# Performance work log

Hardware: AMD Instinct MI355X
Metric: run time of the kernel (lower is better)

## Reference

```python
import jax, jax.numpy as jnp
import numpy as np

N_NODES = 100000
N_REL = 500
DIM = 200
N_EDGES = 200000
T_STEPS = 3
EPS = 1e-12


def _l2norm(x):
    # F.normalize(x): L2 along last dim with eps clamp
    n = jnp.sqrt(jnp.sum(x * x, axis=-1, keepdims=True))
    return x / jnp.maximum(n, EPS)


def _rgcn_layer(h, r, src, rel, dst, W_msg, W_loop):
    # UnionRGCN layer: msg = (h[src] + r[rel]) @ W_msg, mean-aggregated at dst,
    # plus self-loop transform. No activation (active=False), dropout=0.
    msg = (h[src] + r[rel]) @ W_msg                      # [E, D]
    deg = jax.ops.segment_sum(jnp.ones((src.shape[0],), h.dtype), dst,
                              num_segments=N_NODES)       # [N]
    agg = jax.ops.segment_sum(msg, dst, num_segments=N_NODES)
    agg = agg / jnp.maximum(deg, 1.0)[:, None]
    return agg + h @ W_loop


def setup_inputs() -> dict:
    key = jax.random.key(0)
    ks = jax.random.split(key, 10)
    edge_list = []
    for t in range(T_STEPS):
        kt = jax.random.fold_in(ks[0], t)
        k1, k2, k3 = jax.random.split(kt, 3)
        src = jax.random.randint(k1, (N_EDGES,), 0, N_NODES)
        rel = jax.random.randint(k2, (N_EDGES,), 0, N_REL)
        dst = jax.random.randint(k3, (N_EDGES,), 0, N_NODES)
        edge_list.append(jnp.stack([src, rel, dst], axis=1))
    edges = jnp.stack(edge_list)  # [T, E, 3]
    s = 1.0 / np.sqrt(DIM)
    return {
        "edges": edges,
        "entity_embed": jax.random.normal(ks[1], (N_NODES, DIM), jnp.float32),
        "relation_embed": jax.random.normal(ks[2], (N_REL, DIM), jnp.float32),
        "W_msg1": jax.random.normal(ks[3], (DIM, DIM), jnp.float32) * s,
        "W_loop1": jax.random.normal(ks[4], (DIM, DIM), jnp.float32) * s,
        "W_msg2": jax.random.normal(ks[5], (DIM, DIM), jnp.float32) * s,
        "W_loop2": jax.random.normal(ks[6], (DIM, DIM), jnp.float32) * s,
        "time_gate_weight": jax.random.normal(ks[7], (DIM, DIM), jnp.float32) * s * np.sqrt(2.0),
        "time_gate_bias": jnp.zeros((DIM,), jnp.float32),
    }


def reference(edges, entity_embed, relation_embed, W_msg1, W_loop1, W_msg2,
              W_loop2, time_gate_weight, time_gate_bias):
    h = _l2norm(entity_embed)
    r = _l2norm(relation_embed)
    for t in range(T_STEPS):  # small fixed temporal loop, as in source
        src, rel, dst = edges[t, :, 0], edges[t, :, 1], edges[t, :, 2]
        cur = _rgcn_layer(h, r, src, rel, dst, W_msg1, W_loop1)
        cur = _rgcn_layer(cur, r, src, rel, dst, W_msg2, W_loop2)
        cur = _l2norm(cur)
        gate = jax.nn.sigmoid(h @ time_gate_weight + time_gate_bias)
        h = _l2norm(gate * cur + (1.0 - gate) * h)
    return h
```

## Files before the change

kernel.cpp:

```cpp
#include <hip/hip_runtime.h>
#include <math.h>

#define DIMN   200
#define NNODES 100000
#define NREL   500
#define NEDGES 200000
#define KSTEPS 7
#define NB16   16
#define WPK_ELEMS (KSTEPS * NB16 * 64 * 8)
#define SCAN_B 1024
#define NBN    6252
#define FRAG_STRIDE 3584

typedef float  v4f  __attribute__((ext_vector_type(4)));
typedef __bf16 v8bf __attribute__((ext_vector_type(8)));

__device__ __forceinline__ size_t frag_chunk(int nb, int c, int r) {
    return (size_t)(nb * KSTEPS + (c >> 2)) * 512 + (size_t)((c & 3) * 128 + r * 8);
}

__launch_bounds__(256)
__global__ void l2norm_pro(const float* __restrict__ in, __bf16* __restrict__ outR,
                           __bf16* __restrict__ outF, int nrows)
{
    int idx  = blockIdx.x * 256 + threadIdx.x;
    int node = idx >> 5;
    int ch   = idx & 31;
    if (node >= nrows) return;
    float v[8] = {};
    if (ch < 25) {
        const float4* p = (const float4*)(in + (size_t)node * DIMN + ch * 8);
        float4 f0 = p[0], f1 = p[1];
        v[0]=f0.x; v[1]=f0.y; v[2]=f0.z; v[3]=f0.w;
        v[4]=f1.x; v[5]=f1.y; v[6]=f1.z; v[7]=f1.w;
    }
    float ss = 0.0f;
    #pragma unroll
    for (int k = 0; k < 8; ++k) ss += v[k] * v[k];
    #pragma unroll
    for (int off = 16; off; off >>= 1) ss += __shfl_xor(ss, off, 64);
    float s = 1.0f / fmaxf(sqrtf(ss), 1e-12f);
    #pragma unroll
    for (int k = 0; k < 8; ++k) v[k] *= s;
    if (ch < 25) {
        v8bf o;
        #pragma unroll
        for (int k = 0; k < 8; ++k) o[k] = (__bf16)v[k];
        *(v8bf*)(outR + (size_t)node * DIMN + ch * 8) = o;
    }
    if (outF && ch < 28) {
        v8bf o;
        #pragma unroll
        for (int k = 0; k < 8; ++k) o[k] = (ch < 25) ? (__bf16)v[k] : (__bf16)0.0f;
        *(v8bf*)(outF + frag_chunk(node >> 4, ch, node & 15)) = o;
    }
}

__launch_bounds__(256)
__global__ void edge_hist(const int* __restrict__ edges, int* __restrict__ counts, int nedges)
{
    int e = blockIdx.x * 256 + threadIdx.x;
    if (e < nedges) atomicAdd(&counts[edges[e * 3 + 2]], 1);
}

__launch_bounds__(SCAN_B)
__global__ void scan1(const int* __restrict__ counts, int* __restrict__ tmp,
                      int* __restrict__ bsum, int n)
{
    __shared__ int sh[SCAN_B];
    int i = blockIdx.x * SCAN_B + threadIdx.x;
    int v = (i < n) ? counts[i] : 0;
    sh[threadIdx.x] = v;
    __syncthreads();
    for (int off = 1; off < SCAN_B; off <<= 1) {
        int t = (threadIdx.x >= off) ? sh[threadIdx.x - off] : 0;
        __syncthreads();
        sh[threadIdx.x] += t;
        __syncthreads();
    }
    if (i < n) tmp[i] = sh[threadIdx.x];
    if (threadIdx.x == SCAN_B - 1) bsum[blockIdx.x] = sh[threadIdx.x];
}

__launch_bounds__(128)
__global__ void scan2(int* __restrict__ bsum, int nb)
{
    __shared__ int sh[128];
    int v = (threadIdx.x < nb) ? bsum[threadIdx.x] : 0;
    sh[threadIdx.x] = v;
    __syncthreads();
    for (int off = 1; off < 128; off <<= 1) {
        int t = (threadIdx.x >= off) ? sh[threadIdx.x - off] : 0;
        __syncthreads();
        sh[threadIdx.x] += t;
        __syncthreads();
    }
    if (threadIdx.x < nb) bsum[threadIdx.x] = sh[threadIdx.x] - v;
}

__launch_bounds__(SCAN_B)
__global__ void scan3(const int* __restrict__ tmp, const int* __restrict__ bsum,
                      int* __restrict__ offs, int n)
{
    int i = blockIdx.x * SCAN_B + threadIdx.x;
    if (i < n) offs[i + 1] = tmp[i] + bsum[blockIdx.x];
    if (i == 0) offs[0] = 0;
}

__launch_bounds__(256)
__global__ void edge_fill(const int* __restrict__ edges, const int* __restrict__ offs,
                          int* __restrict__ cursor, int2* __restrict__ sorted, int nedges)
{
    int e = blockIdx.x * 256 + threadIdx.x;
    if (e >= nedges) return;
    int s = edges[e * 3 + 0];
    int r = edges[e * 3 + 1];
    int d = edges[e * 3 + 2];
    int p = offs[d] + atomicAdd(&cursor[d], 1);
    sorted[p] = make_int2(s, r);
}

__launch_bounds__(256)
__global__ void agg_S(const int* __restrict__ offs, const int2* __restrict__ sorted,
                      const __bf16* __restrict__ XR, const __bf16* __restrict__ RnR,
                      __bf16* __restrict__ SF, int nnodes)
{
    int wave = (int)((blockIdx.x * blockDim.x + threadIdx.x) >> 6);
    int lane = threadIdx.x & 63;
    if (wave >= nnodes) return;
    int beg = offs[wave], end = offs[wave + 1];
    int ch = lane & 31;
    bool act = ch < 25;

    float acc[8] = {};
    for (int e = beg; e < end; ++e) {
        int2 sr = sorted[e];
        const __bf16* base = (lane < 32) ? (XR + (size_t)sr.x * DIMN)
                                         : (RnR + (size_t)sr.y * DIMN);
        v8bf v = {};
        if (act) v = *(const v8bf*)(base + ch * 8);
        #pragma unroll
        for (int k = 0; k < 8; ++k) acc[k] += (float)v[k];
    }
    #pragma unroll
    for (int k = 0; k < 8; ++k) acc[k] += __shfl_xor(acc[k], 32, 64);

    float rdeg = 1.0f / fmaxf((float)(end - beg), 1.0f);
    if (lane < 32 && ch < 28) {
        v8bf o;
        #pragma unroll
        for (int k = 0; k < 8; ++k) o[k] = act ? (__bf16)(acc[k] * rdeg) : (__bf16)0.0f;
        *(v8bf*)(SF + frag_chunk(wave >> 4, ch, wave & 15)) = o;
    }
}

__launch_bounds__(256)
__global__ void pack_w(const float* __restrict__ W0, const float* __restrict__ W1,
                       const float* __restrict__ W2, const float* __restrict__ W3,
                       const float* __restrict__ W4, __bf16* __restrict__ out)
{
    int id = blockIdx.x * 256 + threadIdx.x;
    const int nchunk = KSTEPS * NB16 * 64;
    if (id >= 5 * nchunk) return;
    int wi = id / nchunk;
    int c  = id % nchunk;
    const float* W = wi == 0 ? W0 : wi == 1 ? W1 : wi == 2 ? W2 : wi == 3 ? W3 : W4;
    int s    = c >> 10;
    int nb   = (c & 1023) >> 6;
    int lane = c & 63;
    int kbase = s * 32 + (lane >> 4) * 8;
    int n     = nb * 16 + (lane & 15);
    __bf16* dst = out + (size_t)wi * WPK_ELEMS + (size_t)c * 8;
    #pragma unroll
    for (int j = 0; j < 8; ++j) {
        int k = kbase + j;
        float v = (k < DIMN && n < DIMN) ? W[k * DIMN + n] : 0.0f;
        dst[j] = (__bf16)v;
    }
}

__launch_bounds__(512)
__global__ void gemm_dual(const __bf16* __restrict__ A1, const __bf16* __restrict__ W1,
                          const __bf16* __restrict__ A2, const __bf16* __restrict__ W2,
                          __bf16* __restrict__ OutR, __bf16* __restrict__ OutF, int M)
{
    const int tid  = threadIdx.x;
    const int w    = tid >> 6;
    const int lane = tid & 63;
    const int rlo  = lane & 15;
    const int g    = lane >> 4;
    const int nb0  = blockIdx.x * 4;
    const int bm   = blockIdx.x * 64;

    __shared__ __bf16 T[64][264];

    v4f acc[4][2];
    #pragma unroll
    for (int mi = 0; mi < 4; ++mi)
        #pragma unroll
        for (int ni = 0; ni < 2; ++ni)
            acc[mi][ni] = (v4f){0.f, 0.f, 0.f, 0.f};

    const __bf16* w1b = W1 + (size_t)(w * 2 * 64 + lane) * 8;
    const __bf16* w2b = W2 + (size_t)(w * 2 * 64 + lane) * 8;

    #pragma unroll
    for (int s = 0; s < KSTEPS; ++s) {
        v8bf b1[2], b2[2];
        #pragma unroll
        for (int ni = 0; ni < 2; ++ni) {
            size_t bo = ((size_t)s * NB16 * 64 + ni * 64) * 8;
            b1[ni] = *(const v8bf*)(w1b + bo);
            b2[ni] = *(const v8bf*)(w2b + bo);
        }
        #pragma unroll
        for (int mi = 0; mi < 4; ++mi) {
            size_t aoff = (size_t)((nb0 + mi) * KSTEPS + s) * 512 + lane * 8;
            v8bf a1 = *(const v8bf*)(A1 + aoff);
            v8bf a2 = *(const v8bf*)(A2 + aoff);
            #pragma unroll
            for (int ni = 0; ni < 2; ++ni)
                acc[mi][ni] = __builtin_amdgcn_mfma_f32_16x16x32_bf16(a1, b1[ni], acc[mi][ni], 0, 0, 0);
            #pragma unroll
            for (int ni = 0; ni < 2; ++ni)
                acc[mi][ni] = __builtin_amdgcn_mfma_f32_16x16x32_bf16(a2, b2[ni], acc[mi][ni], 0, 0, 0);
        }
    }

    #pragma unroll
    for (int mi = 0; mi < 4; ++mi)
        #pragma unroll
        for (int reg = 0; reg < 4; ++reg)
            #pragma unroll
            for (int ni = 0; ni < 2; ++ni)
                T[mi * 16 + g * 4 + reg][w * 32 + ni * 16 + rlo] = (__bf16)acc[mi][ni][reg];
    __syncthreads();

    #pragma unroll
    for (int j = 0; j < 4; ++j) {
        int it = tid + j * 512;
        if (it < 1792) {
            int slot = it & 63;
            int q = it >> 6;
            int s = q % 7, nb = q / 7;
            *(v8bf*)(OutF + (size_t)((nb0 + nb) * KSTEPS + s) * 512 + slot * 8) =
                *(const v8bf*)&T[nb * 16 + (slot & 15)][s * 32 + (slot >> 4) * 8];
        }
    }
    #pragma unroll
    for (int j = 0; j < 4; ++j) {
        int it = tid + j * 512;
        if (it < 1600) {
            int row = it / 25, ch = it - row * 25;
            int gr = bm + row;
            if (gr < M)
                *(v8bf*)(OutR + (size_t)gr * DIMN + ch * 8) = *(const v8bf*)&T[row][ch * 8];
        }
    }
}

__launch_bounds__(512)
__global__ void gemm_mega(const __bf16* __restrict__ A1, const __bf16* __restrict__ W1,
                          const __bf16* __restrict__ A2, const __bf16* __restrict__ W2,
                          const __bf16* __restrict__ A3, const __bf16* __restrict__ W3,
                          const float* __restrict__ Bias,
                          __bf16* __restrict__ HR, __bf16* __restrict__ HF,
                          float* __restrict__ DoutF, int M, int finalStep)
{
    const int tid  = threadIdx.x;
    const int w    = tid >> 6;
    const int lane = tid & 63;
    const int rlo  = lane & 15;
    const int g    = lane >> 4;
    const int nb0  = blockIdx.x * 2;
    const int bm   = blockIdx.x * 32;

    __shared__ __bf16 As[42][512];
    __shared__ float  rsq1[32][8];
    __shared__ float  rsq2[32][8];
    __bf16 (*T)[264] = (__bf16(*)[264])&As[0][0];

    v4f acc1[2][2], acc2[2][2];
    #pragma unroll
    for (int mi = 0; mi < 2; ++mi)
        #pragma unroll
        for (int ni = 0; ni < 2; ++ni) {
            acc1[mi][ni] = (v4f){0.f, 0.f, 0.f, 0.f};
            acc2[mi][ni] = (v4f){0.f, 0.f, 0.f, 0.f};
        }

    #pragma unroll
    for (int j = 0; j < 6; ++j) {
        int c = w + j * 8;
        if (c < 42) {
            int stream = c / 14;
            int rem    = c - stream * 14;
            int nb     = rem / 7;
            int s      = rem - nb * 7;
            const __bf16* Asrc = stream == 0 ? A1 : stream == 1 ? A2 : A3;
            *(v8bf*)&As[c][lane * 8] =
                *(const v8bf*)(Asrc + (size_t)((nb0 + nb) * KSTEPS + s) * 512 + lane * 8);
        }
    }

    const __bf16* w1b = W1 + (size_t)(w * 2 * 64 + lane) * 8;
    const __bf16* w2b = W2 + (size_t)(w * 2 * 64 + lane) * 8;
    const __bf16* w3b = W3 + (size_t)(w * 2 * 64 + lane) * 8;
    __syncthreads();

    #pragma unroll
    for (int s = 0; s < KSTEPS; ++s) {
        v8bf b1[2], b2[2], b3[2];
        #pragma unroll
        for (int ni = 0; ni < 2; ++ni) {
            size_t bo = ((size_t)s * NB16 * 64 + ni * 64) * 8;
            b1[ni] = *(const v8bf*)(w1b + bo);
            b2[ni] = *(const v8bf*)(w2b + bo);
            b3[ni] = *(const v8bf*)(w3b + bo);
        }
        #pragma unroll
        for (int mi = 0; mi < 2; ++mi) {
            v8bf a1 = *(const v8bf*)&As[ 0 + mi * 7 + s][lane * 8];
            v8bf a2 = *(const v8bf*)&As[14 + mi * 7 + s][lane * 8];
            v8bf a3 = *(const v8bf*)&As[28 + mi * 7 + s][lane * 8];
            #pragma unroll
            for (int ni = 0; ni < 2; ++ni)
                acc1[mi][ni] = __builtin_amdgcn_mfma_f32_16x16x32_bf16(a1, b1[ni], acc1[mi][ni], 0, 0, 0);
            #pragma unroll
            for (int ni = 0; ni < 2; ++ni)
                acc1[mi][ni] = __builtin_amdgcn_mfma_f32_16x16x32_bf16(a2, b2[ni], acc1[mi][ni], 0, 0, 0);
            #pragma unroll
            for (int ni = 0; ni < 2; ++ni)
                acc2[mi][ni] = __builtin_amdgcn_mfma_f32_16x16x32_bf16(a3, b3[ni], acc2[mi][ni], 0, 0, 0);
        }
    }

    #pragma unroll
    for (int mi = 0; mi < 2; ++mi)
        #pragma unroll
        for (int reg = 0; reg < 4; ++reg) {
            float ss = 0.0f;
            #pragma unroll
            for (int ni = 0; ni < 2; ++ni) ss += acc1[mi][ni][reg] * acc1[mi][ni][reg];
            ss += __shfl_xor(ss, 1, 64);
            ss += __shfl_xor(ss, 2, 64);
            ss += __shfl_xor(ss, 4, 64);
            ss += __shfl_xor(ss, 8, 64);
            if (rlo == 0) rsq1[mi * 16 + g * 4 + reg][w] = ss;
        }
    __syncthreads();

    #pragma unroll
    for (int j = 0; j < 2; ++j) {
        int it = tid + j * 512;
        if (it < 800) {
            int row = it / 25, ch = it - row * 25;
            int gr = bm + row;
            v8bf hv = {};
            if (gr < M) hv = *(const v8bf*)(HR + (size_t)gr * DIMN + ch * 8);
            *(v8bf*)&T[row][ch * 8] = hv;
        }
    }
    __syncthreads();

    #pragma unroll
    for (int mi = 0; mi < 2; ++mi)
        #pragma unroll
        for (int reg = 0; reg < 4; ++reg) {
            int rl = mi * 16 + g * 4 + reg;
            float tot = rsq1[rl][0] + rsq1[rl][1] + rsq1[rl][2] + rsq1[rl][3]
                      + rsq1[rl][4] + rsq1[rl][5] + rsq1[rl][6] + rsq1[rl][7];
            float sc1 = 1.0f / fmaxf(sqrtf(tot), 1e-12f);
            float ss = 0.0f;
            #pragma unroll
            for (int ni = 0; ni < 2; ++ni) {
                int c = w * 32 + ni * 16 + rlo;
                float v = 0.0f;
                if (c < DIMN) {
                    float cur = acc1[mi][ni][reg] * sc1;
                    float gg  = 1.0f / (1.0f + __expf(-(acc2[mi][ni][reg] + Bias[c])));
                    float hh  = (float)T[rl][c];
                    v = gg * cur + (1.0f - gg) * hh;
                }
                acc1[mi][ni][reg] = v;
                ss += v * v;
            }
            ss += __shfl_xor(ss, 1, 64);
            ss += __shfl_xor(ss, 2, 64);
            ss += __shfl_xor(ss, 4, 64);
            ss += __shfl_xor(ss, 8, 64);
            if (rlo == 0) rsq2[rl][w] = ss;
        }
    __syncthreads();

    #pragma unroll
    for (int mi = 0; mi < 2; ++mi)
        #pragma unroll
        for (int reg = 0; reg < 4; ++reg) {
            int rl = mi * 16 + g * 4 + reg;
            float tot = rsq2[rl][0] + rsq2[rl][1] + rsq2[rl][2] + rsq2[rl][3]
                      + rsq2[rl][4] + rsq2[rl][5] + rsq2[rl][6] + rsq2[rl][7];
            float sc2 = 1.0f / fmaxf(sqrtf(tot), 1e-12f);
            #pragma unroll
            for (int ni = 0; ni < 2; ++ni) {
                int c = w * 32 + ni * 16 + rlo;
                T[rl][c] = (__bf16)(acc1[mi][ni][reg] * sc2);
            }
        }
    __syncthreads();

    if (!finalStep) {
        #pragma unroll
        for (int j = 0; j < 2; ++j) {
            int it = tid + j * 512;
            if (it < 800) {
                int row = it / 25, ch = it - row * 25;
                int gr = bm + row;
                if (gr < M)
                    *(v8bf*)(HR + (size_t)gr * DIMN + ch * 8) = *(const v8bf*)&T[row][ch * 8];
            }
        }
        #pragma unroll
        for (int j = 0; j < 2; ++j) {
            int it = tid + j * 512;
            if (it < 896) {
                int slot = it & 63;
                int q = it >> 6;
                int s = q % 7, nb = q / 7;
                *(v8bf*)(HF + (size_t)((nb0 + nb) * KSTEPS + s) * 512 + slot * 8) =
                    *(const v8bf*)&T[nb * 16 + (slot & 15)][s * 32 + (slot >> 4) * 8];
            }
        }
    } else {
        #pragma unroll
        for (int j = 0; j < 2; ++j) {
            int it = tid + j * 512;
            if (it < 800) {
                int row = it / 25, ch = it - row * 25;
                int gr = bm + row;
                if (gr < M) {
                    v8bf o = *(const v8bf*)&T[row][ch * 8];
                    float4* q0 = (float4*)(DoutF + (size_t)gr * DIMN + ch * 8);
                    q0[0] = make_float4((float)o[0], (float)o[1], (float)o[2], (float)o[3]);
                    q0[1] = make_float4((float)o[4], (float)o[5], (float)o[6], (float)o[7]);
                }
            }
        }
    }
}

extern "C" void kernel_launch(void* const* d_in, const int* in_sizes, int n_in,
                              void* d_out, int out_size, void* d_ws, size_t ws_size,
                              hipStream_t stream)
{
    const int*   edges = (const int*)  d_in[0];
    const float* ent   = (const float*)d_in[1];
    const float* relE  = (const float*)d_in[2];
    const float* Wm1   = (const float*)d_in[3];
    const float* Wl1   = (const float*)d_in[4];
    const float* Wm2   = (const float*)d_in[5];
    const float* Wl2   = (const float*)d_in[6];
    const float* Wtg   = (const float*)d_in[7];
    const float* bias  = (const float*)d_in[8];
    float* Dout = (float*)d_out;

    const size_t NM    = (size_t)NNODES * DIMN;
    const size_t FRAGN = (size_t)NBN * FRAG_STRIDE;

    __bf16* hR   = (__bf16*)d_ws;
    __bf16* hF   = hR + NM;
    __bf16* SF   = hF + FRAGN;
    __bf16* BR   = SF + FRAGN;
    __bf16* BF   = BR + NM;
    __bf16* RnR  = BF + FRAGN;
    __bf16* Wpk  = RnR + (size_t)NREL * DIMN;
    __bf16* pWm1 = Wpk + 0 * (size_t)WPK_ELEMS;
    __bf16* pWl1 = Wpk + 1 * (size_t)WPK_ELEMS;
    __bf16* pWm2 = Wpk + 2 * (size_t)WPK_ELEMS;
    __bf16* pWl2 = Wpk + 3 * (size_t)WPK_ELEMS;
    __bf16* pWtg = Wpk + 4 * (size_t)WPK_ELEMS;
    int*  counts = (int*)(Wpk + 5 * (size_t)WPK_ELEMS);
    int2* sorted = (int2*)(counts + NNODES);
    int*  offs   = (int*)(sorted + NEDGES);
    int*  bsum   = offs + (NNODES + 1);
    int*  stmp   = bsum + 256;

    dim3 blk(256);
    const int GD = (NNODES + 63) / 64;
    const int GM = (NNODES + 31) / 32;
    dim3 ngrid32((NNODES * 32 + 255) / 256);
    dim3 rgrid32((NREL * 32 + 255) / 256);
    dim3 agrid((NNODES + 3) / 4);
    dim3 egrid((NEDGES + 255) / 256);
    const int NSB = (NNODES + SCAN_B - 1) / SCAN_B;

    pack_w<<<dim3((5 * KSTEPS * NB16 * 64 + 255) / 256), blk, 0, stream>>>(Wm1, Wl1, Wm2, Wl2, Wtg, Wpk);
    l2norm_pro<<<ngrid32, blk, 0, stream>>>(ent, hR, hF, NNODES);
    l2norm_pro<<<rgrid32, blk, 0, stream>>>(relE, RnR, nullptr, NREL);

    for (int t = 0; t < 3; ++t) {
        const int* ed = edges + (size_t)t * NEDGES * 3;
        hipMemsetAsync(counts, 0, NNODES * sizeof(int), stream);
        edge_hist<<<egrid, blk, 0, stream>>>(ed, counts, NEDGES);
        scan1<<<NSB, SCAN_B, 0, stream>>>(counts, stmp, bsum, NNODES);
        scan2<<<1, 128, 0, stream>>>(bsum, NSB);
        scan3<<<NSB, SCAN_B, 0, stream>>>(stmp, bsum, offs, NNODES);
        hipMemsetAsync(counts, 0, NNODES * sizeof(int), stream);
        edge_fill<<<egrid, blk, 0, stream>>>(ed, offs, counts, sorted, NEDGES);
        agg_S<<<agrid, blk, 0, stream>>>(offs, sorted, hR, RnR, SF, NNODES);
        gemm_dual<<<GD, dim3(512), 0, stream>>>(SF, pWm1, hF, pWl1, BR, BF, NNODES);
        agg_S<<<agrid, blk, 0, stream>>>(offs, sorted, BR, RnR, SF, NNODES);
        gemm_mega<<<GM, dim3(512), 0, stream>>>(SF, pWm2, BF, pWl2, hF, pWtg, bias,
                                                hR, hF, Dout, NNODES, (t == 2) ? 1 : 0);
    }
}
```

Measured before the change: 994.7 us.

## Batch CSR construction for all timesteps and drop LDS staging in gemm_mega

The per-timestep histogram, scan and fill kernels are replaced by a single pass over all three timesteps. It uses one combined offset array and is indexed per step, which removes about 15 launches and memsets. Separately, gemm_mega no longer stages the A fragments in a 42x512 LDS buffer and loads them straight from global memory. That cuts LDS use and one barrier, which may raise occupancy, but A loads now hit global/cache directly and the K loop is no longer force-unrolled. Removing the barrier before T is reused is safe only because T no longer aliases As.

```diff
diff --git a/kernel.cpp b/kernel.cpp
--- a/kernel.cpp
+++ b/kernel.cpp
@@ -5,6 +5,7 @@
 #define NNODES 100000
 #define NREL   500
 #define NEDGES 200000
+#define TSTEPS 3
 #define KSTEPS 7
 #define NB16   16
 #define WPK_ELEMS (KSTEPS * NB16 * 64 * 8)
@@ -57,10 +58,13 @@
 }
 
 __launch_bounds__(256)
-__global__ void edge_hist(const int* __restrict__ edges, int* __restrict__ counts, int nedges)
+__global__ void edge_hist3(const int* __restrict__ edges, int* __restrict__ counts)
 {
     int e = blockIdx.x * 256 + threadIdx.x;
-    if (e < nedges) atomicAdd(&counts[edges[e * 3 + 2]], 1);
+    if (e < TSTEPS * NEDGES) {
+        int t = e / NEDGES;
+        atomicAdd(&counts[t * NNODES + edges[(size_t)e * 3 + 2]], 1);
+    }
 }
 
 __launch_bounds__(SCAN_B)
@@ -82,14 +86,14 @@
     if (threadIdx.x == SCAN_B - 1) bsum[blockIdx.x] = sh[threadIdx.x];
 }
 
-__launch_bounds__(128)
+__launch_bounds__(SCAN_B)
 __global__ void scan2(int* __restrict__ bsum, int nb)
 {
-    __shared__ int sh[128];
+    __shared__ int sh[SCAN_B];
     int v = (threadIdx.x < nb) ? bsum[threadIdx.x] : 0;
     sh[threadIdx.x] = v;
     __syncthreads();
-    for (int off = 1; off < 128; off <<= 1) {
+    for (int off = 1; off < SCAN_B; off <<= 1) {
         int t = (threadIdx.x >= off) ? sh[threadIdx.x - off] : 0;
         __syncthreads();
         sh[threadIdx.x] += t;
@@ -108,15 +112,17 @@
 }
 
 __launch_bounds__(256)
-__global__ void edge_fill(const int* __restrict__ edges, const int* __restrict__ offs,
-                          int* __restrict__ cursor, int2* __restrict__ sorted, int nedges)
+__global__ void edge_fill3(const int* __restrict__ edges, const int* __restrict__ offs,
+                           int* __restrict__ cursor, int2* __restrict__ sorted)
 {
     int e = blockIdx.x * 256 + threadIdx.x;
-    if (e >= nedges) return;
-    int s = edges[e * 3 + 0];
-    int r = edges[e * 3 + 1];
-    int d = edges[e * 3 + 2];
-    int p = offs[d] + atomicAdd(&cursor[d], 1);
+    if (e >= TSTEPS * NEDGES) return;
+    int t = e / NEDGES;
+    int s = edges[(size_t)e * 3 + 0];
+    int r = edges[(size_t)e * 3 + 1];
+    int d = edges[(size_t)e * 3 + 2];
+    int sn = t * NNODES + d;
+    int p = offs[sn] + atomicAdd(&cursor[sn], 1);
     sorted[p] = make_int2(s, r);
 }
 
@@ -275,10 +281,9 @@
     const int nb0  = blockIdx.x * 2;
     const int bm   = blockIdx.x * 32;
 
-    __shared__ __bf16 As[42][512];
+    __shared__ __bf16 T[32][264];
     __shared__ float  rsq1[32][8];
     __shared__ float  rsq2[32][8];
-    __bf16 (*T)[264] = (__bf16(*)[264])&As[0][0];
 
     v4f acc1[2][2], acc2[2][2];
     #pragma unroll
@@ -289,26 +294,10 @@
             acc2[mi][ni] = (v4f){0.f, 0.f, 0.f, 0.f};
         }
 
-    #pragma unroll
-    for (int j = 0; j < 6; ++j) {
-        int c = w + j * 8;
-        if (c < 42) {
-            int stream = c / 14;
-            int rem    = c - stream * 14;
-            int nb     = rem / 7;
-            int s      = rem - nb * 7;
-            const __bf16* Asrc = stream == 0 ? A1 : stream == 1 ? A2 : A3;
-            *(v8bf*)&As[c][lane * 8] =
-                *(const v8bf*)(Asrc + (size_t)((nb0 + nb) * KSTEPS + s) * 512 + lane * 8);
-        }
-    }
-
     const __bf16* w1b = W1 + (size_t)(w * 2 * 64 + lane) * 8;
     const __bf16* w2b = W2 + (size_t)(w * 2 * 64 + lane) * 8;
     const __bf16* w3b = W3 + (size_t)(w * 2 * 64 + lane) * 8;
-    __syncthreads();
-
-    #pragma unroll
+
     for (int s = 0; s < KSTEPS; ++s) {
         v8bf b1[2], b2[2], b3[2];
         #pragma unroll
@@ -320,9 +309,10 @@
         }
         #pragma unroll
         for (int mi = 0; mi < 2; ++mi) {
-            v8bf a1 = *(const v8bf*)&As[ 0 + mi * 7 + s][lane * 8];
-            v8bf a2 = *(const v8bf*)&As[14 + mi * 7 + s][lane * 8];
-            v8bf a3 = *(const v8bf*)&As[28 + mi * 7 + s][lane * 8];
+            size_t aoff = (size_t)((nb0 + mi) * KSTEPS + s) * 512 + lane * 8;
+            v8bf a1 = *(const v8bf*)(A1 + aoff);
+            v8bf a2 = *(const v8bf*)(A2 + aoff);
+            v8bf a3 = *(const v8bf*)(A3 + aoff);
             #pragma unroll
             for (int ni = 0; ni < 2; ++ni)
                 acc1[mi][ni] = __builtin_amdgcn_mfma_f32_16x16x32_bf16(a1, b1[ni], acc1[mi][ni], 0, 0, 0);
@@ -348,8 +338,6 @@
             ss += __shfl_xor(ss, 8, 64);
             if (rlo == 0) rsq1[mi * 16 + g * 4 + reg][w] = ss;
         }
-    __syncthreads();
-
     #pragma unroll
     for (int j = 0; j < 2; ++j) {
         int it = tid + j * 512;
@@ -480,10 +468,11 @@
     __bf16* pWl2 = Wpk + 3 * (size_t)WPK_ELEMS;
     __bf16* pWtg = Wpk + 4 * (size_t)WPK_ELEMS;
     int*  counts = (int*)(Wpk + 5 * (size_t)WPK_ELEMS);
-    int2* sorted = (int2*)(counts + NNODES);
-    int*  offs   = (int*)(sorted + NEDGES);
-    int*  bsum   = offs + (NNODES + 1);
-    int*  stmp   = bsum + 256;
+    int*  cursor = counts + TSTEPS * NNODES;
+    int2* sorted = (int2*)(cursor + TSTEPS * NNODES);
+    int*  offs   = (int*)(sorted + TSTEPS * NEDGES);
+    int*  bsum   = offs + (TSTEPS * NNODES + 1);
+    int*  stmp   = bsum + SCAN_B;
 
     dim3 blk(256);
     const int GD = (NNODES + 63) / 64;
@@ -491,25 +480,26 @@
     dim3 ngrid32((NNODES * 32 + 255) / 256);
     dim3 rgrid32((NREL * 32 + 255) / 256);
     dim3 agrid((NNODES + 3) / 4);
-    dim3 egrid((NEDGES + 255) / 256);
-    const int NSB = (NNODES + SCAN_B - 1) / SCAN_B;
+    dim3 egrid3((TSTEPS * NEDGES + 255) / 256);
+    const int NTOT = TSTEPS * NNODES;
+    const int NSB  = (NTOT + SCAN_B - 1) / SCAN_B;
 
     pack_w<<<dim3((5 * KSTEPS * NB16 * 64 + 255) / 256), blk, 0, stream>>>(Wm1, Wl1, Wm2, Wl2, Wtg, Wpk);
     l2norm_pro<<<ngrid32, blk, 0, stream>>>(ent, hR, hF, NNODES);
     l2norm_pro<<<rgrid32, blk, 0, stream>>>(relE, RnR, nullptr, NREL);
 
+    hipMemsetAsync(counts, 0, 2 * NTOT * sizeof(int), stream);
+    edge_hist3<<<egrid3, blk, 0, stream>>>(edges, counts);
+    scan1<<<NSB, SCAN_B, 0, stream>>>(counts, stmp, bsum, NTOT);
+    scan2<<<1, SCAN_B, 0, stream>>>(bsum, NSB);
+    scan3<<<NSB, SCAN_B, 0, stream>>>(stmp, bsum, offs, NTOT);
+    edge_fill3<<<egrid3, blk, 0, stream>>>(edges, offs, cursor, sorted);
+
     for (int t = 0; t < 3; ++t) {
-        const int* ed = edges + (size_t)t * NEDGES * 3;
-        hipMemsetAsync(counts, 0, NNODES * sizeof(int), stream);
-        edge_hist<<<egrid, blk, 0, stream>>>(ed, counts, NEDGES);
-        scan1<<<NSB, SCAN_B, 0, stream>>>(counts, stmp, bsum, NNODES);
-        scan2<<<1, 128, 0, stream>>>(bsum, NSB);
-        scan3<<<NSB, SCAN_B, 0, stream>>>(stmp, bsum, offs, NNODES);
-        hipMemsetAsync(counts, 0, NNODES * sizeof(int), stream);
-        edge_fill<<<egrid, blk, 0, stream>>>(ed, offs, counts, sorted, NEDGES);
-        agg_S<<<agrid, blk, 0, stream>>>(offs, sorted, hR, RnR, SF, NNODES);
+        const int* offsT = offs + (size_t)t * NNODES;
+        agg_S<<<agrid, blk, 0, stream>>>(offsT, sorted, hR, RnR, SF, NNODES);
         gemm_dual<<<GD, dim3(512), 0, stream>>>(SF, pWm1, hF, pWl1, BR, BF, NNODES);
-        agg_S<<<agrid, blk, 0, stream>>>(offs, sorted, BR, RnR, SF, NNODES);
+        agg_S<<<agrid, blk, 0, stream>>>(offsT, sorted, BR, RnR, SF, NNODES);
         gemm_mega<<<GM, dim3(512), 0, stream>>>(SF, pWm2, BF, pWl2, hF, pWtg, bias,
                                                 hR, hF, Dout, NNODES, (t == 2) ? 1 : 0);
     }
```

Result: faster. 967.3 us (-2.8%).
